# Optimization experiments

Measured on AMD Instinct MI355X. Metric: run time of the kernel, lower is better.

The kernel has to match this reference:

```python
import jax, jax.numpy as jnp
import numpy as np
from jax import lax

NMS_SIZE = 5
THR = 0.0
B, C, H, W = 8, 1, 2048, 2048
# fixed capacity for the jit-compatible nonzero (padded with -1); generous upper
# bound on number of surviving local maxima (~HW/25 per map, half above thr=0)
MAX_KEYPOINTS = 2_000_000


def setup_inputs() -> dict:
    key = jax.random.key(0)
    scores = jax.random.normal(key, (B, C, H, W), dtype=jnp.float32)
    return {"scores": scores}


def _local_max(scores):
    # MaxPool2d(kernel=5, stride=1, padding=2) == SAME-padded windowed max
    return lax.reduce_window(
        scores,
        -jnp.inf,
        lax.max,
        window_dimensions=(1, 1, NMS_SIZE, NMS_SIZE),
        window_strides=(1, 1, 1, 1),
        padding="SAME",
    )


def reference(scores):
    maxima = (scores == _local_max(scores)) & (scores > THR)  # [B,C,H,W] bool
    # torch: maxima.nonzero().t()[2:4] -> (row, col) coordinates of survivors.
    # jit-compatible fixed-size nonzero, padded with -1 (extra entries beyond
    # the true count are fill values, matching a compacted index list).
    _, _, hh, ww = jnp.nonzero(maxima, size=MAX_KEYPOINTS, fill_value=-1)
    return jnp.stack([hh, ww])  # [2, MAX_KEYPOINTS] int
```

## Files before the change

### kernel.cpp

```cpp
#include <hip/hip_runtime.h>
#include <stdint.h>
#include <math.h>

#define BATCH 8
#define HH 2048
#define WW 2048
#define R 8
#define NSTRIPS (HH / R)
#define NBLK (NSTRIPS * BATCH)
#define BLK_WORDS (R * WW / 32)
#define MAXK 2000000
#define TAIL_I4 (MAXK / 4)
#define TAIL_PER_BLK ((TAIL_I4 + NBLK - 1) / NBLK)

__global__ __launch_bounds__(256) void nms_mask(const float* __restrict__ scores,
                                                uint8_t* __restrict__ maskbytes,
                                                int* __restrict__ counts) {
    const int chunk = (int)(blockIdx.x % 8) * (NBLK / 8) + (int)(blockIdx.x / 8);

    const int tid  = threadIdx.x;
    const int lane = tid & 63;
    const int wv   = tid >> 6;
    const int b     = chunk >> 8;
    const int strip = chunk & (NSTRIPS - 1);
    const int h0    = strip * R;
    const int c0    = wv * 512 + lane * 8;
    const float* colp = scores + (size_t)b * HH * WW + c0;
    const bool has_l = (c0 != 0);
    const bool has_r = (c0 != WW - 8);

    float win[5][12];

#define LOAD_ROW(PH, hrow)                                                    \
    do {                                                                      \
        const int h_ = (hrow);                                                \
        if ((unsigned)h_ < (unsigned)HH) {                                    \
            const float* p_ = colp + (size_t)h_ * WW;                         \
            float4 a_ = *(const float4*)(p_);                                 \
            float4 b_ = *(const float4*)(p_ + 4);                             \
            win[PH][2] = a_.x; win[PH][3] = a_.y;                             \
            win[PH][4] = a_.z; win[PH][5] = a_.w;                             \
            win[PH][6] = b_.x; win[PH][7] = b_.y;                             \
            win[PH][8] = b_.z; win[PH][9] = b_.w;                             \
            if (has_l) {                                                      \
                float2 hl_ = *(const float2*)(p_ - 2);                        \
                win[PH][0] = hl_.x; win[PH][1] = hl_.y;                       \
            } else { win[PH][0] = -INFINITY; win[PH][1] = -INFINITY; }        \
            if (has_r) {                                                      \
                float2 hr_ = *(const float2*)(p_ + 8);                        \
                win[PH][10] = hr_.x; win[PH][11] = hr_.y;                     \
            } else { win[PH][10] = -INFINITY; win[PH][11] = -INFINITY; }      \
        } else {                                                              \
            _Pragma("unroll")                                                 \
            for (int k_ = 0; k_ < 12; ++k_) win[PH][k_] = -INFINITY;          \
        }                                                                     \
    } while (0)

    LOAD_ROW(0, h0 - 2);
    LOAD_ROW(1, h0 - 1);
    LOAD_ROW(2, h0 + 0);
    LOAD_ROW(3, h0 + 1);

    int pc = 0;
    size_t outbyte = (((size_t)(b * HH + h0) * WW) + c0) >> 3;

#pragma unroll
    for (int i = 0; i < R; ++i) {
        LOAD_ROW((4 + i) % 5, h0 + 2 + i);
        const int CEN = (2 + i) % 5;

        float v[12];
#pragma unroll
        for (int k = 0; k < 12; ++k)
            v[k] = fmaxf(fmaxf(fmaxf(win[0][k], win[1][k]),
                               fmaxf(win[2][k], win[3][k])), win[4][k]);
        float p[11];
#pragma unroll
        for (int k = 0; k < 11; ++k) p[k] = fmaxf(v[k], v[k + 1]);

        uint32_t byte = 0;
#pragma unroll
        for (int j = 0; j < 8; ++j) {
            const float hm = fmaxf(fmaxf(p[j], p[j + 2]), v[j + 4]);
            const float s  = win[CEN][j + 2];
            if ((s == hm) && (s > 0.0f)) byte |= (1u << j);
        }
        maskbytes[outbyte] = (uint8_t)byte;
        outbyte += WW / 8;
        pc += __popc(byte);
    }
#undef LOAD_ROW

#pragma unroll
    for (int d = 32; d >= 1; d >>= 1) pc += __shfl_down(pc, d, 64);
    __shared__ int wsum[4];
    if (lane == 0) wsum[wv] = pc;
    __syncthreads();
    if (tid == 0) counts[chunk] = wsum[0] + wsum[1] + wsum[2] + wsum[3];
}

__global__ __launch_bounds__(256) void compact(const uint32_t* __restrict__ bitmask,
                                               const int* __restrict__ counts,
                                               int* __restrict__ out_h,
                                               int* __restrict__ out_w) {
    const int chunk = (int)blockIdx.x;
    const int tid   = threadIdx.x;
    const int lane  = tid & 63, wv = tid >> 6;

    const uint4 ca = ((const uint4*)counts)[2 * tid];
    const uint4 cb = ((const uint4*)counts)[2 * tid + 1];
    const int i0 = tid * 8;
    int contrib = 0, full = 0;
    {
        const uint32_t cv[8] = {ca.x, ca.y, ca.z, ca.w, cb.x, cb.y, cb.z, cb.w};
#pragma unroll
        for (int j = 0; j < 8; ++j) {
            full += (int)cv[j];
            contrib += (i0 + j < chunk) ? (int)cv[j] : 0;
        }
    }

    int rA = contrib, rB = full;
#pragma unroll
    for (int d = 32; d >= 1; d >>= 1) {
        rA += __shfl_down(rA, d, 64);
        rB += __shfl_down(rB, d, 64);
    }
    __shared__ int wsA[4], wsB[4], wscan[4];
    if (lane == 0) { wsA[wv] = rA; wsB[wv] = rB; }

    const uint2 m = ((const uint2*)(bitmask + (size_t)chunk * BLK_WORDS))[tid];
    const int pc = __popc(m.x) + __popc(m.y);

    int incl = pc;
#pragma unroll
    for (int d = 1; d < 64; d <<= 1) {
        int n = __shfl_up(incl, d, 64);
        if (lane >= d) incl += n;
    }
    if (lane == 63) wscan[wv] = incl;
    __syncthreads();

    const int chunk_base = wsA[0] + wsA[1] + wsA[2] + wsA[3];
    int total = wsB[0] + wsB[1] + wsB[2] + wsB[3];
    if (total > MAXK) total = MAXK;
    int wbase = 0;
    for (int i = 0; i < wv; ++i) wbase += wscan[i];

    const int h0 = (chunk & (NSTRIPS - 1)) * R;
    int off = chunk_base + wbase + (incl - pc);

    uint32_t words[2] = {m.x, m.y};
    const uint32_t local0 = (uint32_t)tid * 64u;
#pragma unroll
    for (int wj = 0; wj < 2; ++wj) {
        uint32_t mm = words[wj];
        const uint32_t lb = local0 + (uint32_t)wj * 32u;
        while (mm) {
            const int bit = __ffs(mm) - 1;
            mm &= mm - 1;
            const uint32_t L = lb + (uint32_t)bit;
            if (off < MAXK) {
                out_h[off] = h0 + (int)(L >> 11);
                out_w[off] = (int)(L & 2047u);
            }
            ++off;
        }
    }

    const int i4base = chunk * TAIL_PER_BLK;
    for (int t = tid; t < TAIL_PER_BLK; t += 256) {
        const int i4 = i4base + t;
        if (i4 >= TAIL_I4) break;
        const int base = i4 * 4;
        if (base + 4 <= total) continue;
        if (base >= total) {
            const int4 neg = make_int4(-1, -1, -1, -1);
            *(int4*)(out_h + base) = neg;
            *(int4*)(out_w + base) = neg;
        } else {
#pragma unroll
            for (int j = 0; j < 4; ++j) {
                const int idx = base + j;
                if (idx >= total) { out_h[idx] = -1; out_w[idx] = -1; }
            }
        }
    }
}

extern "C" void kernel_launch(void* const* d_in, const int* in_sizes, int n_in,
                              void* d_out, int out_size, void* d_ws, size_t ws_size,
                              hipStream_t stream) {
    const float* scores = (const float*)d_in[0];
    int* out = (int*)d_out;

    uint32_t* bitmask = (uint32_t*)d_ws;
    int* counts = (int*)((char*)d_ws + (size_t)NBLK * BLK_WORDS * 4);

    nms_mask<<<NBLK, 256, 0, stream>>>(scores, (uint8_t*)bitmask, counts);
    compact<<<NBLK, 256, 0, stream>>>(bitmask, counts, out, out + MAXK);
}
```

Before: 46.00 us.

## Retile mask kernel to 4 columns per thread and 16-row strips

After: 55.95 us. +21.6%, slower.

```diff
diff --git a/kernel.cpp b/kernel.cpp
--- a/kernel.cpp
+++ b/kernel.cpp
@@ -5,31 +5,35 @@
 #define BATCH 8
 #define HH 2048
 #define WW 2048
-#define R 8
+#define R 16
 #define NSTRIPS (HH / R)
-#define NBLK (NSTRIPS * BATCH)
+#define HALF_W 1024
+#define NBLK1 (BATCH * NSTRIPS * 2)
+#define NBLK2 (BATCH * NSTRIPS)
 #define BLK_WORDS (R * WW / 32)
 #define MAXK 2000000
 #define TAIL_I4 (MAXK / 4)
-#define TAIL_PER_BLK ((TAIL_I4 + NBLK - 1) / NBLK)
-
-__global__ __launch_bounds__(256) void nms_mask(const float* __restrict__ scores,
-                                                uint8_t* __restrict__ maskbytes,
-                                                int* __restrict__ counts) {
-    const int chunk = (int)(blockIdx.x % 8) * (NBLK / 8) + (int)(blockIdx.x / 8);
-
+#define TAIL_PER_BLK ((TAIL_I4 + NBLK2 - 1) / NBLK2)
+
+__global__ __launch_bounds__(256, 8) void nms_mask(const float* __restrict__ scores,
+                                                   uint8_t* __restrict__ maskbytes,
+                                                   int* __restrict__ counts) {
+    const int bid  = (int)blockIdx.x;
     const int tid  = threadIdx.x;
     const int lane = tid & 63;
     const int wv   = tid >> 6;
-    const int b     = chunk >> 8;
-    const int strip = chunk & (NSTRIPS - 1);
+
+    const int b     = bid >> 8;
+    const int rem   = bid & 255;
+    const int strip = rem >> 1;
+    const int half  = rem & 1;
     const int h0    = strip * R;
-    const int c0    = wv * 512 + lane * 8;
+    const int c0    = half * HALF_W + tid * 4;
     const float* colp = scores + (size_t)b * HH * WW + c0;
     const bool has_l = (c0 != 0);
-    const bool has_r = (c0 != WW - 8);
-
-    float win[5][12];
+    const bool has_r = (c0 != WW - 4);
+
+    float win[5][8];
 
 #define LOAD_ROW(PH, hrow)                                                    \
     do {                                                                      \
@@ -37,22 +41,19 @@
         if ((unsigned)h_ < (unsigned)HH) {                                    \
             const float* p_ = colp + (size_t)h_ * WW;                         \
             float4 a_ = *(const float4*)(p_);                                 \
-            float4 b_ = *(const float4*)(p_ + 4);                             \
             win[PH][2] = a_.x; win[PH][3] = a_.y;                             \
             win[PH][4] = a_.z; win[PH][5] = a_.w;                             \
-            win[PH][6] = b_.x; win[PH][7] = b_.y;                             \
-            win[PH][8] = b_.z; win[PH][9] = b_.w;                             \
             if (has_l) {                                                      \
                 float2 hl_ = *(const float2*)(p_ - 2);                        \
                 win[PH][0] = hl_.x; win[PH][1] = hl_.y;                       \
             } else { win[PH][0] = -INFINITY; win[PH][1] = -INFINITY; }        \
             if (has_r) {                                                      \
-                float2 hr_ = *(const float2*)(p_ + 8);                        \
-                win[PH][10] = hr_.x; win[PH][11] = hr_.y;                     \
-            } else { win[PH][10] = -INFINITY; win[PH][11] = -INFINITY; }      \
+                float2 hr_ = *(const float2*)(p_ + 4);                        \
+                win[PH][6] = hr_.x; win[PH][7] = hr_.y;                       \
+            } else { win[PH][6] = -INFINITY; win[PH][7] = -INFINITY; }        \
         } else {                                                              \
             _Pragma("unroll")                                                 \
-            for (int k_ = 0; k_ < 12; ++k_) win[PH][k_] = -INFINITY;          \
+            for (int k_ = 0; k_ < 8; ++k_) win[PH][k_] = -INFINITY;           \
         }                                                                     \
     } while (0)
 
@@ -62,32 +63,35 @@
     LOAD_ROW(3, h0 + 1);
 
     int pc = 0;
-    size_t outbyte = (((size_t)(b * HH + h0) * WW) + c0) >> 3;
+    size_t outbyte = (((size_t)(b * HH + h0) * WW) >> 3) + (size_t)(half * 128 + (tid >> 1));
+    const bool store_lane = ((lane & 1) == 0);
 
 #pragma unroll
     for (int i = 0; i < R; ++i) {
         LOAD_ROW((4 + i) % 5, h0 + 2 + i);
         const int CEN = (2 + i) % 5;
 
-        float v[12];
-#pragma unroll
-        for (int k = 0; k < 12; ++k)
+        float v[8];
+#pragma unroll
+        for (int k = 0; k < 8; ++k)
             v[k] = fmaxf(fmaxf(fmaxf(win[0][k], win[1][k]),
                                fmaxf(win[2][k], win[3][k])), win[4][k]);
-        float p[11];
-#pragma unroll
-        for (int k = 0; k < 11; ++k) p[k] = fmaxf(v[k], v[k + 1]);
-
-        uint32_t byte = 0;
-#pragma unroll
-        for (int j = 0; j < 8; ++j) {
+        float p[7];
+#pragma unroll
+        for (int k = 0; k < 7; ++k) p[k] = fmaxf(v[k], v[k + 1]);
+
+        uint32_t nib = 0;
+#pragma unroll
+        for (int j = 0; j < 4; ++j) {
             const float hm = fmaxf(fmaxf(p[j], p[j + 2]), v[j + 4]);
             const float s  = win[CEN][j + 2];
-            if ((s == hm) && (s > 0.0f)) byte |= (1u << j);
-        }
-        maskbytes[outbyte] = (uint8_t)byte;
+            if ((s == hm) && (s > 0.0f)) nib |= (1u << j);
+        }
+        pc += __popc(nib);
+
+        const uint32_t other = __shfl_down(nib, 1, 64);
+        if (store_lane) maskbytes[outbyte] = (uint8_t)(nib | (other << 4));
         outbyte += WW / 8;
-        pc += __popc(byte);
     }
 #undef LOAD_ROW
 
@@ -96,7 +100,7 @@
     __shared__ int wsum[4];
     if (lane == 0) wsum[wv] = pc;
     __syncthreads();
-    if (tid == 0) counts[chunk] = wsum[0] + wsum[1] + wsum[2] + wsum[3];
+    if (tid == 0) counts[bid] = wsum[0] + wsum[1] + wsum[2] + wsum[3];
 }
 
 __global__ __launch_bounds__(256) void compact(const uint32_t* __restrict__ bitmask,
@@ -106,6 +110,7 @@
     const int chunk = (int)blockIdx.x;
     const int tid   = threadIdx.x;
     const int lane  = tid & 63, wv = tid >> 6;
+    const int lim   = 2 * chunk;
 
     const uint4 ca = ((const uint4*)counts)[2 * tid];
     const uint4 cb = ((const uint4*)counts)[2 * tid + 1];
@@ -116,7 +121,7 @@
 #pragma unroll
         for (int j = 0; j < 8; ++j) {
             full += (int)cv[j];
-            contrib += (i0 + j < chunk) ? (int)cv[j] : 0;
+            contrib += (i0 + j < lim) ? (int)cv[j] : 0;
         }
     }
 
@@ -129,8 +134,8 @@
     __shared__ int wsA[4], wsB[4], wscan[4];
     if (lane == 0) { wsA[wv] = rA; wsB[wv] = rB; }
 
-    const uint2 m = ((const uint2*)(bitmask + (size_t)chunk * BLK_WORDS))[tid];
-    const int pc = __popc(m.x) + __popc(m.y);
+    const uint4 m = ((const uint4*)(bitmask + (size_t)chunk * BLK_WORDS))[tid];
+    const int pc = __popc(m.x) + __popc(m.y) + __popc(m.z) + __popc(m.w);
 
     int incl = pc;
 #pragma unroll
@@ -150,10 +155,10 @@
     const int h0 = (chunk & (NSTRIPS - 1)) * R;
     int off = chunk_base + wbase + (incl - pc);
 
-    uint32_t words[2] = {m.x, m.y};
-    const uint32_t local0 = (uint32_t)tid * 64u;
-#pragma unroll
-    for (int wj = 0; wj < 2; ++wj) {
+    uint32_t words[4] = {m.x, m.y, m.z, m.w};
+    const uint32_t local0 = (uint32_t)tid * 128u;
+#pragma unroll
+    for (int wj = 0; wj < 4; ++wj) {
         uint32_t mm = words[wj];
         const uint32_t lb = local0 + (uint32_t)wj * 32u;
         while (mm) {
@@ -195,8 +200,8 @@
     int* out = (int*)d_out;
 
     uint32_t* bitmask = (uint32_t*)d_ws;
-    int* counts = (int*)((char*)d_ws + (size_t)NBLK * BLK_WORDS * 4);
-
-    nms_mask<<<NBLK, 256, 0, stream>>>(scores, (uint8_t*)bitmask, counts);
-    compact<<<NBLK, 256, 0, stream>>>(bitmask, counts, out, out + MAXK);
+    int* counts = (int*)((char*)d_ws + (size_t)NBLK2 * BLK_WORDS * 4);
+
+    nms_mask<<<NBLK1, 256, 0, stream>>>(scores, (uint8_t*)bitmask, counts);
+    compact<<<NBLK2, 256, 0, stream>>>(bitmask, counts, out, out + MAXK);
 }
```
